# Performance work log

Hardware: AMD Instinct MI355X
Metric: run time of the kernel (lower is better)

The kernel has to match this reference:

```python
import jax, jax.numpy as jnp
import numpy as np
import math

B, T, E, H = 4, 1024, 1024, 16
D = E // H  # head_dim = 64
EPS = 1e-5


def setup_inputs() -> dict:
    key = jax.random.key(0)
    k1, k2, k3 = jax.random.split(key, 3)
    x = jax.random.normal(k1, (B, T, E), dtype=jnp.float32)
    scale = jnp.ones((E,), dtype=jnp.float32)
    w_qkv = jax.random.normal(k2, (3 * E, E), dtype=jnp.float32) * (1.0 / math.sqrt(E))
    w_proj = jax.random.normal(k3, (E, E), dtype=jnp.float32) * (1.0 / math.sqrt(E))
    return {"x": x, "scale": scale, "w_qkv": w_qkv, "w_proj": w_proj}


def reference(x, scale, w_qkv, w_proj):
    # RMSNorm
    xn = x * jax.lax.rsqrt(jnp.mean(x * x, axis=-1, keepdims=True) + EPS) * scale
    # QKV projection (torch Linear: y = x @ W.T)
    qkv = jnp.einsum('bte,fe->btf', xn, w_qkv)  # [B,T,3E]
    q, k, v = jnp.split(qkv, 3, axis=-1)
    # [B,T,E] -> [B,H,T,D]
    q = q.reshape(B, T, H, D).transpose(0, 2, 1, 3)
    k = k.reshape(B, T, H, D).transpose(0, 2, 1, 3)
    v = v.reshape(B, T, H, D).transpose(0, 2, 1, 3)
    # causal attention
    attn = jnp.einsum('bhqd,bhkd->bhqk', q, k) / math.sqrt(D)
    causal = jnp.tril(jnp.ones((T, T), dtype=bool))
    attn = jnp.where(causal, attn, -jnp.inf)
    attn = jax.nn.softmax(attn, axis=-1)
    out = jnp.einsum('bhqk,bhkd->bhqd', attn, v)  # [B,H,T,D]
    out = out.transpose(0, 2, 1, 3).reshape(B, T, E)
    # output projection
    return jnp.einsum('bte,fe->btf', out, w_proj)
```

## Files before the change

### kernel.cpp

```cpp
#include <hip/hip_runtime.h>
#include <hip/hip_bf16.h>
#include <stdint.h>

#define B_SZ 4
#define T_SEQ 1024
#define E_DIM 1024
#define NH 16
#define HD 64
#define THREE_E 3072
#define NTOK 4096

typedef unsigned short u16;
typedef unsigned int u32;
using short8v = __attribute__((ext_vector_type(8))) short;
using short4v = __attribute__((ext_vector_type(4))) short;
using f32x4 = __attribute__((ext_vector_type(4))) float;

__device__ __forceinline__ u16 f2bf(float f) {
    union { float f; uint32_t u; } c; c.f = f;
    uint32_t u = c.u;
    uint32_t r = (u + 0x7FFFu + ((u >> 16) & 1u)) >> 16;
    return (u16)r;
}

__device__ __forceinline__ u32 cvt_pk_bf16(float lo, float hi) {
    u32 r;
    asm("v_cvt_pk_bf16_f32 %0, %1, %2" : "=v"(r) : "v"(lo), "v"(hi));
    return r;
}

__device__ __forceinline__ void gload_lds16(const u16* g, u16* l) {
    __builtin_amdgcn_global_load_lds((const __attribute__((address_space(1))) void*)g,
                                     (__attribute__((address_space(3))) void*)l, 16, 0, 0);
}

__global__ __launch_bounds__(256) void rmsnorm_kernel(const float* __restrict__ x,
                                                      const float* __restrict__ scale,
                                                      u16* __restrict__ xn) {
    int row = blockIdx.x;
    int tid = threadIdx.x;
    const float4* xr = reinterpret_cast<const float4*>(x + (size_t)row * E_DIM);
    float4 v = xr[tid];
    float ss = v.x * v.x + v.y * v.y + v.z * v.z + v.w * v.w;
    for (int off = 32; off > 0; off >>= 1) ss += __shfl_xor(ss, off);
    __shared__ float red[4];
    if ((tid & 63) == 0) red[tid >> 6] = ss;
    __syncthreads();
    float total = red[0] + red[1] + red[2] + red[3];
    float rs = rsqrtf(total * (1.0f / E_DIM) + 1e-5f);
    const float4* sc4 = reinterpret_cast<const float4*>(scale);
    float4 s = sc4[tid];
    u16* o = xn + (size_t)row * E_DIM + tid * 4;
    o[0] = f2bf(v.x * rs * s.x);
    o[1] = f2bf(v.y * rs * s.y);
    o[2] = f2bf(v.z * rs * s.z);
    o[3] = f2bf(v.w * rs * s.w);
}

__global__ __launch_bounds__(256) void cast_weights_kernel(const float* __restrict__ wq,
                                                           const float* __restrict__ wp,
                                                           u16* __restrict__ wqb,
                                                           u16* __restrict__ wpb) {
    const int NQ = (THREE_E * E_DIM) / 4;
    const int NP = (E_DIM * E_DIM) / 4;
    int i = blockIdx.x * 256 + threadIdx.x;
    if (i < NQ) {
        float4 v = reinterpret_cast<const float4*>(wq)[i];
        u16* o = wqb + (size_t)i * 4;
        o[0] = f2bf(v.x); o[1] = f2bf(v.y); o[2] = f2bf(v.z); o[3] = f2bf(v.w);
    } else if (i < NQ + NP) {
        int j = i - NQ;
        float4 v = reinterpret_cast<const float4*>(wp)[j];
        u16* o = wpb + (size_t)j * 4;
        o[0] = f2bf(v.x); o[1] = f2bf(v.y); o[2] = f2bf(v.z); o[3] = f2bf(v.w);
    }
}

template <bool OUT_BF16>
__global__ __launch_bounds__(256) void gemm_lds_kernel(const u16* __restrict__ A,
                                                       const u16* __restrict__ Bw,
                                                       void* __restrict__ C,
                                                       int N, int K) {
    __shared__ u16 As[128 * 64];
    __shared__ u16 Bs[128 * 64];
    int tid = threadIdx.x;
    int lane = tid & 63, wid = tid >> 6;
    int lq = lane & 15, lg = lane >> 4;

    int gx = gridDim.x;
    int nwg = gx * gridDim.y;
    int orig = blockIdx.y * gx + blockIdx.x;
    int cpx = nwg >> 3;
    int swz = (orig & 7) * cpx + (orig >> 3);
    int bx = swz % gx, by = swz / gx;
    int mblk = by * 128, nblk = bx * 128;

    int srow = wid * 32 + (lane >> 3);
    int csw = ((lane & 7) ^ ((lane >> 3) & 7)) * 8;
    const u16* gA = A + (size_t)(mblk + srow) * K + csw;
    const u16* gB = Bw + (size_t)(nblk + srow) * K + csw;
    u16* lA = As + wid * 2048;
    u16* lB = Bs + wid * 2048;

    f32x4 acc[4][4] = {};
    int m0w = (wid >> 1) * 64;
    int n0w = (wid & 1) * 64;
    int r7 = lq & 7;

    for (int k0 = 0; k0 < K; k0 += 64) {
        __syncthreads();
#pragma unroll
        for (int i = 0; i < 4; ++i) gload_lds16(gA + k0 + (size_t)i * 8 * K, lA + i * 512);
#pragma unroll
        for (int i = 0; i < 4; ++i) gload_lds16(gB + k0 + (size_t)i * 8 * K, lB + i * 512);
        __syncthreads();
        short8v af[2][4], bf[2][4];
#pragma unroll
        for (int kk = 0; kk < 2; ++kk) {
#pragma unroll
            for (int mi = 0; mi < 4; ++mi)
                af[kk][mi] = *reinterpret_cast<const short8v*>(
                    &As[(m0w + mi * 16 + lq) * 64 + ((kk * 4 + lg) ^ r7) * 8]);
#pragma unroll
            for (int ni = 0; ni < 4; ++ni)
                bf[kk][ni] = *reinterpret_cast<const short8v*>(
                    &Bs[(n0w + ni * 16 + lq) * 64 + ((kk * 4 + lg) ^ r7) * 8]);
        }
        __builtin_amdgcn_s_setprio(1);
#pragma unroll
        for (int mi = 0; mi < 4; ++mi)
#pragma unroll
            for (int ni = 0; ni < 4; ++ni) {
                acc[mi][ni] = __builtin_amdgcn_mfma_f32_16x16x32_bf16(af[0][mi], bf[0][ni], acc[mi][ni], 0, 0, 0);
                acc[mi][ni] = __builtin_amdgcn_mfma_f32_16x16x32_bf16(af[1][mi], bf[1][ni], acc[mi][ni], 0, 0, 0);
            }
        __builtin_amdgcn_s_setprio(0);
    }
#pragma unroll
    for (int mi = 0; mi < 4; ++mi) {
#pragma unroll
        for (int ni = 0; ni < 4; ++ni) {
#pragma unroll
            for (int j = 0; j < 4; ++j) {
                int row = mblk + m0w + mi * 16 + lg * 4 + j;
                int col = nblk + n0w + ni * 16 + lq;
                float val = acc[mi][ni][j];
                if (OUT_BF16)
                    ((u16*)C)[(size_t)row * N + col] = f2bf(val);
                else
                    ((float*)C)[(size_t)row * N + col] = val;
            }
        }
    }
}

template <bool DIAG>
__device__ __forceinline__ void attn_tile(const u16 (*__restrict__ Kt)[72],
                                          const u16 (*__restrict__ Vt)[72],
                                          const short8v* __restrict__ qf,
                                          f32x4* __restrict__ o,
                                          float& l_r,
                                          int lq, int lg, int wid, int kt64, int qg) {
    const float CLOG = 0.18033688011112042f;
    const float MOFF = 11.541560327111707f;
    int ksmax = DIAG ? wid : 3;
    f32x4 st[4] = {};
    __builtin_amdgcn_s_setprio(1);
#pragma unroll
    for (int ks = 0; ks < 4; ++ks) {
        if (ks <= ksmax) {
            short8v a0 = *reinterpret_cast<const short8v*>(&Kt[ks * 16 + lq][lg * 8]);
            short8v a1 = *reinterpret_cast<const short8v*>(&Kt[ks * 16 + lq][32 + lg * 8]);
            st[ks] = __builtin_amdgcn_mfma_f32_16x16x32_bf16(a0, qf[0], st[ks], 0, 0, 0);
            st[ks] = __builtin_amdgcn_mfma_f32_16x16x32_bf16(a1, qf[1], st[ks], 0, 0, 0);
        }
    }
    __builtin_amdgcn_s_setprio(0);
    float p[4][4];
    float psum = 0.f;
#pragma unroll
    for (int ks = 0; ks < 4; ++ks)
#pragma unroll
        for (int j = 0; j < 4; ++j) {
            float v = st[ks][j];
            if (DIAG) {
                int kg = kt64 + ks * 16 + lg * 4 + j;
                v = (ks <= ksmax && kg <= qg) ? v : -INFINITY;
            }
            float pv = exp2f(fmaf(v, CLOG, -MOFF));
            p[ks][j] = pv;
            psum += pv;
        }
    l_r += psum;
    union { u32 w2[2]; short4v v; } pa[4];
#pragma unroll
    for (int ks = 0; ks < 4; ++ks) {
        pa[ks].w2[0] = cvt_pk_bf16(p[ks][0], p[ks][1]);
        pa[ks].w2[1] = cvt_pk_bf16(p[ks][2], p[ks][3]);
    }
    __builtin_amdgcn_s_setprio(1);
#pragma unroll
    for (int ni = 0; ni < 4; ++ni) {
        int d = ni * 16 + lq;
        int sw = ((d >> 3) & 7) << 3;
        const u16* vrow = Vt[d];
#pragma unroll
        for (int ks = 0; ks < 4; ++ks) {
            if (ks <= ksmax) {
                short4v vb = *reinterpret_cast<const short4v*>(&vrow[(ks * 16 + lg * 4) ^ sw]);
                o[ni] = __builtin_amdgcn_mfma_f32_16x16x16bf16_1k(pa[ks].v, vb, o[ni], 0, 0, 0);
            }
        }
    }
    __builtin_amdgcn_s_setprio(0);
}

__global__ __launch_bounds__(256) void attn_kernel(const u16* __restrict__ qkv,
                                                   u16* __restrict__ out) {
    int tid = threadIdx.x;
    int lane = tid & 63, wid = tid >> 6;
    int lq = lane & 15, lg = lane >> 4;
    int bh = blockIdx.y;
    int b = bh >> 4, h = bh & 15;
    int qlo_blk = blockIdx.x;
    int qhi_blk = 15 - qlo_blk;
    int qt_lo = qlo_blk * 64 + wid * 16;
    int qt_hi = qhi_blk * 64 + wid * 16;

    const u16* base = qkv + (size_t)b * T_SEQ * THREE_E;
    const u16* Qb = base + h * HD;
    const u16* Kb = base + E_DIM + h * HD;

    __shared__ __align__(16) u16 Kt[2][64][72];
    __shared__ __align__(16) u16 Vt[2][64][72];

    short8v qf_lo[2], qf_hi[2];
    {
        const u16* qr = Qb + (size_t)(qt_lo + lq) * THREE_E + lg * 8;
        qf_lo[0] = *reinterpret_cast<const short8v*>(qr);
        qf_lo[1] = *reinterpret_cast<const short8v*>(qr + 32);
        qr = Qb + (size_t)(qt_hi + lq) * THREE_E + lg * 8;
        qf_hi[0] = *reinterpret_cast<const short8v*>(qr);
        qf_hi[1] = *reinterpret_cast<const short8v*>(qr + 32);
    }
    f32x4 o_lo[4] = {}, o_hi[4] = {};
    float l_lo = 0.f, l_hi = 0.f;
    int qg_lo = qt_lo + lq, qg_hi = qt_hi + lq;

    int row_s = tid >> 3, c8 = tid & 7;
    short8v kreg[2], vreg[2];

#pragma unroll
    for (int i = 0; i < 2; ++i) {
        const u16* src = Kb + (size_t)(row_s + i * 32) * THREE_E + c8 * 8;
        kreg[i] = *reinterpret_cast<const short8v*>(src);
        vreg[i] = *reinterpret_cast<const short8v*>(src + E_DIM);
    }
#pragma unroll
    for (int i = 0; i < 2; ++i) {
        int row = row_s + i * 32;
        *reinterpret_cast<short8v*>(&Kt[0][row][c8 * 8]) = kreg[i];
        int rs = row ^ (c8 << 3);
#pragma unroll
        for (int e = 0; e < 8; ++e) Vt[0][c8 * 8 + e][rs] = (u16)vreg[i][e];
    }
    if (qhi_blk >= 1) {
#pragma unroll
        for (int i = 0; i < 2; ++i) {
            const u16* src = Kb + (size_t)(64 + row_s + i * 32) * THREE_E + c8 * 8;
            kreg[i] = *reinterpret_cast<const short8v*>(src);
            vreg[i] = *reinterpret_cast<const short8v*>(src + E_DIM);
        }
    }
    __syncthreads();

    for (int kt = 0; kt <= qhi_blk; ++kt) {
        int cur = kt & 1;
        if (kt < qhi_blk) {
#pragma unroll
            for (int i = 0; i < 2; ++i) {
                int row = row_s + i * 32;
                *reinterpret_cast<short8v*>(&Kt[cur ^ 1][row][c8 * 8]) = kreg[i];
                int rs = row ^ (c8 << 3);
#pragma unroll
                for (int e = 0; e < 8; ++e) Vt[cur ^ 1][c8 * 8 + e][rs] = (u16)vreg[i][e];
            }
            if (kt + 1 < qhi_blk) {
#pragma unroll
                for (int i = 0; i < 2; ++i) {
                    const u16* src = Kb + (size_t)((kt + 2) * 64 + row_s + i * 32) * THREE_E + c8 * 8;
                    kreg[i] = *reinterpret_cast<const short8v*>(src);
                    vreg[i] = *reinterpret_cast<const short8v*>(src + E_DIM);
                }
            }
        }
        if (kt < qlo_blk)
            attn_tile<false>(Kt[cur], Vt[cur], qf_lo, o_lo, l_lo, lq, lg, wid, kt * 64, qg_lo);
        else if (kt == qlo_blk)
            attn_tile<true>(Kt[cur], Vt[cur], qf_lo, o_lo, l_lo, lq, lg, wid, kt * 64, qg_lo);
        if (kt < qhi_blk)
            attn_tile<false>(Kt[cur], Vt[cur], qf_hi, o_hi, l_hi, lq, lg, wid, kt * 64, qg_hi);
        else
            attn_tile<true>(Kt[cur], Vt[cur], qf_hi, o_hi, l_hi, lq, lg, wid, kt * 64, qg_hi);
        __syncthreads();
    }
    float lf_lo = l_lo, lf_hi = l_hi;
    lf_lo += __shfl_xor(lf_lo, 16); lf_lo += __shfl_xor(lf_lo, 32);
    lf_hi += __shfl_xor(lf_hi, 16); lf_hi += __shfl_xor(lf_hi, 32);
#pragma unroll
    for (int j = 0; j < 4; ++j) {
        float linv = 1.0f / __shfl(lf_lo, lg * 4 + j);
        size_t row = (size_t)b * T_SEQ + qt_lo + lg * 4 + j;
#pragma unroll
        for (int ni = 0; ni < 4; ++ni)
            out[row * E_DIM + h * HD + ni * 16 + lq] = f2bf(o_lo[ni][j] * linv);
    }
#pragma unroll
    for (int j = 0; j < 4; ++j) {
        float linv = 1.0f / __shfl(lf_hi, lg * 4 + j);
        size_t row = (size_t)b * T_SEQ + qt_hi + lg * 4 + j;
#pragma unroll
        for (int ni = 0; ni < 4; ++ni)
            out[row * E_DIM + h * HD + ni * 16 + lq] = f2bf(o_hi[ni][j] * linv);
    }
}

extern "C" void kernel_launch(void* const* d_in, const int* in_sizes, int n_in,
                              void* d_out, int out_size, void* d_ws, size_t ws_size,
                              hipStream_t stream) {
    const float* x = (const float*)d_in[0];
    const float* scale = (const float*)d_in[1];
    const float* w_qkv = (const float*)d_in[2];
    const float* w_proj = (const float*)d_in[3];
    float* out = (float*)d_out;

    char* ws = (char*)d_ws;
    u16* xn   = (u16*)(ws);
    u16* wqb  = (u16*)(ws + (8ull << 20));
    u16* wpb  = (u16*)(ws + (14ull << 20));
    u16* qkv  = (u16*)(ws + (16ull << 20));
    u16* aout = (u16*)(ws + (40ull << 20));

    rmsnorm_kernel<<<dim3(NTOK), dim3(256), 0, stream>>>(x, scale, xn);
    cast_weights_kernel<<<dim3(4096), dim3(256), 0, stream>>>(w_qkv, w_proj, wqb, wpb);
    gemm_lds_kernel<true><<<dim3(THREE_E / 128, NTOK / 128), dim3(256), 0, stream>>>(
        xn, wqb, (void*)qkv, THREE_E, E_DIM);
    attn_kernel<<<dim3(8, B_SZ * NH), dim3(256), 0, stream>>>(qkv, aout);
    gemm_lds_kernel<false><<<dim3(E_DIM / 128, NTOK / 128), dim3(256), 0, stream>>>(
        aout, wpb, (void*)out, E_DIM, E_DIM);
}
```

Measured before the change: 98.49 us.

## Fuse prep kernels, split attention across 8 waves, narrow proj GEMM tile

Result: faster. 89.67 us (-9.0%).

```diff
diff --git a/kernel.cpp b/kernel.cpp
--- a/kernel.cpp
+++ b/kernel.cpp
@@ -34,55 +34,57 @@
                                      (__attribute__((address_space(3))) void*)l, 16, 0, 0);
 }
 
-__global__ __launch_bounds__(256) void rmsnorm_kernel(const float* __restrict__ x,
-                                                      const float* __restrict__ scale,
-                                                      u16* __restrict__ xn) {
-    int row = blockIdx.x;
+__global__ __launch_bounds__(256) void prep_kernel(const float* __restrict__ x,
+                                                   const float* __restrict__ scale,
+                                                   const float* __restrict__ wq,
+                                                   const float* __restrict__ wp,
+                                                   u16* __restrict__ xn,
+                                                   u16* __restrict__ wqb,
+                                                   u16* __restrict__ wpb) {
+    int bx = blockIdx.x;
     int tid = threadIdx.x;
-    const float4* xr = reinterpret_cast<const float4*>(x + (size_t)row * E_DIM);
-    float4 v = xr[tid];
-    float ss = v.x * v.x + v.y * v.y + v.z * v.z + v.w * v.w;
-    for (int off = 32; off > 0; off >>= 1) ss += __shfl_xor(ss, off);
-    __shared__ float red[4];
-    if ((tid & 63) == 0) red[tid >> 6] = ss;
-    __syncthreads();
-    float total = red[0] + red[1] + red[2] + red[3];
-    float rs = rsqrtf(total * (1.0f / E_DIM) + 1e-5f);
-    const float4* sc4 = reinterpret_cast<const float4*>(scale);
-    float4 s = sc4[tid];
-    u16* o = xn + (size_t)row * E_DIM + tid * 4;
-    o[0] = f2bf(v.x * rs * s.x);
-    o[1] = f2bf(v.y * rs * s.y);
-    o[2] = f2bf(v.z * rs * s.z);
-    o[3] = f2bf(v.w * rs * s.w);
-}
-
-__global__ __launch_bounds__(256) void cast_weights_kernel(const float* __restrict__ wq,
-                                                           const float* __restrict__ wp,
-                                                           u16* __restrict__ wqb,
-                                                           u16* __restrict__ wpb) {
-    const int NQ = (THREE_E * E_DIM) / 4;
-    const int NP = (E_DIM * E_DIM) / 4;
-    int i = blockIdx.x * 256 + threadIdx.x;
-    if (i < NQ) {
-        float4 v = reinterpret_cast<const float4*>(wq)[i];
-        u16* o = wqb + (size_t)i * 4;
-        o[0] = f2bf(v.x); o[1] = f2bf(v.y); o[2] = f2bf(v.z); o[3] = f2bf(v.w);
-    } else if (i < NQ + NP) {
-        int j = i - NQ;
-        float4 v = reinterpret_cast<const float4*>(wp)[j];
-        u16* o = wpb + (size_t)j * 4;
-        o[0] = f2bf(v.x); o[1] = f2bf(v.y); o[2] = f2bf(v.z); o[3] = f2bf(v.w);
-    }
-}
-
-template <bool OUT_BF16>
+    if (bx < 4096) {
+        int row = bx;
+        const float4* xr = reinterpret_cast<const float4*>(x + (size_t)row * E_DIM);
+        float4 v = xr[tid];
+        float ss = v.x * v.x + v.y * v.y + v.z * v.z + v.w * v.w;
+        for (int off = 32; off > 0; off >>= 1) ss += __shfl_xor(ss, off);
+        __shared__ float red[4];
+        if ((tid & 63) == 0) red[tid >> 6] = ss;
+        __syncthreads();
+        float total = red[0] + red[1] + red[2] + red[3];
+        float rs = rsqrtf(total * (1.0f / E_DIM) + 1e-5f);
+        float4 s = reinterpret_cast<const float4*>(scale)[tid];
+        u16* o = xn + (size_t)row * E_DIM + tid * 4;
+        o[0] = f2bf(v.x * rs * s.x);
+        o[1] = f2bf(v.y * rs * s.y);
+        o[2] = f2bf(v.z * rs * s.z);
+        o[3] = f2bf(v.w * rs * s.w);
+    } else {
+        const int NQ = (THREE_E * E_DIM) / 4;
+        const int NP = (E_DIM * E_DIM) / 4;
+        int i = (bx - 4096) * 256 + tid;
+        if (i < NQ) {
+            float4 v = reinterpret_cast<const float4*>(wq)[i];
+            u16* o = wqb + (size_t)i * 4;
+            o[0] = f2bf(v.x); o[1] = f2bf(v.y); o[2] = f2bf(v.z); o[3] = f2bf(v.w);
+        } else if (i < NQ + NP) {
+            int j = i - NQ;
+            float4 v = reinterpret_cast<const float4*>(wp)[j];
+            u16* o = wpb + (size_t)j * 4;
+            o[0] = f2bf(v.x); o[1] = f2bf(v.y); o[2] = f2bf(v.z); o[3] = f2bf(v.w);
+        }
+    }
+}
+
+template <int BN, bool OUT_BF16>
 __global__ __launch_bounds__(256) void gemm_lds_kernel(const u16* __restrict__ A,
                                                        const u16* __restrict__ Bw,
                                                        void* __restrict__ C,
                                                        int N, int K) {
+    constexpr int NFR = BN / 32;
     __shared__ u16 As[128 * 64];
-    __shared__ u16 Bs[128 * 64];
+    __shared__ u16 Bs[BN * 64];
     int tid = threadIdx.x;
     int lane = tid & 63, wid = tid >> 6;
     int lq = lane & 15, lg = lane >> 4;
@@ -93,18 +95,19 @@
     int cpx = nwg >> 3;
     int swz = (orig & 7) * cpx + (orig >> 3);
     int bx = swz % gx, by = swz / gx;
-    int mblk = by * 128, nblk = bx * 128;
-
-    int srow = wid * 32 + (lane >> 3);
+    int mblk = by * 128, nblk = bx * BN;
+
+    int srowA = wid * 32 + (lane >> 3);
+    int srowB = wid * (BN / 4) + (lane >> 3);
     int csw = ((lane & 7) ^ ((lane >> 3) & 7)) * 8;
-    const u16* gA = A + (size_t)(mblk + srow) * K + csw;
-    const u16* gB = Bw + (size_t)(nblk + srow) * K + csw;
+    const u16* gA = A + (size_t)(mblk + srowA) * K + csw;
+    const u16* gB = Bw + (size_t)(nblk + srowB) * K + csw;
     u16* lA = As + wid * 2048;
-    u16* lB = Bs + wid * 2048;
-
-    f32x4 acc[4][4] = {};
+    u16* lB = Bs + wid * (BN / 4) * 64;
+
+    f32x4 acc[4][NFR] = {};
     int m0w = (wid >> 1) * 64;
-    int n0w = (wid & 1) * 64;
+    int n0w = (wid & 1) * (BN / 2);
     int r7 = lq & 7;
 
     for (int k0 = 0; k0 < K; k0 += 64) {
@@ -112,9 +115,9 @@
 #pragma unroll
         for (int i = 0; i < 4; ++i) gload_lds16(gA + k0 + (size_t)i * 8 * K, lA + i * 512);
 #pragma unroll
-        for (int i = 0; i < 4; ++i) gload_lds16(gB + k0 + (size_t)i * 8 * K, lB + i * 512);
+        for (int i = 0; i < NFR; ++i) gload_lds16(gB + k0 + (size_t)i * 8 * K, lB + i * 512);
         __syncthreads();
-        short8v af[2][4], bf[2][4];
+        short8v af[2][4], bf[2][NFR];
 #pragma unroll
         for (int kk = 0; kk < 2; ++kk) {
 #pragma unroll
@@ -122,7 +125,7 @@
                 af[kk][mi] = *reinterpret_cast<const short8v*>(
                     &As[(m0w + mi * 16 + lq) * 64 + ((kk * 4 + lg) ^ r7) * 8]);
 #pragma unroll
-            for (int ni = 0; ni < 4; ++ni)
+            for (int ni = 0; ni < NFR; ++ni)
                 bf[kk][ni] = *reinterpret_cast<const short8v*>(
                     &Bs[(n0w + ni * 16 + lq) * 64 + ((kk * 4 + lg) ^ r7) * 8]);
         }
@@ -130,7 +133,7 @@
 #pragma unroll
         for (int mi = 0; mi < 4; ++mi)
 #pragma unroll
-            for (int ni = 0; ni < 4; ++ni) {
+            for (int ni = 0; ni < NFR; ++ni) {
                 acc[mi][ni] = __builtin_amdgcn_mfma_f32_16x16x32_bf16(af[0][mi], bf[0][ni], acc[mi][ni], 0, 0, 0);
                 acc[mi][ni] = __builtin_amdgcn_mfma_f32_16x16x32_bf16(af[1][mi], bf[1][ni], acc[mi][ni], 0, 0, 0);
             }
@@ -139,7 +142,7 @@
 #pragma unroll
     for (int mi = 0; mi < 4; ++mi) {
 #pragma unroll
-        for (int ni = 0; ni < 4; ++ni) {
+        for (int ni = 0; ni < NFR; ++ni) {
 #pragma unroll
             for (int j = 0; j < 4; ++j) {
                 int row = mblk + m0w + mi * 16 + lg * 4 + j;
@@ -160,10 +163,10 @@
                                           const short8v* __restrict__ qf,
                                           f32x4* __restrict__ o,
                                           float& l_r,
-                                          int lq, int lg, int wid, int kt64, int qg) {
+                                          int lq, int lg, int w4, int kt64, int qg) {
     const float CLOG = 0.18033688011112042f;
     const float MOFF = 11.541560327111707f;
-    int ksmax = DIAG ? wid : 3;
+    int ksmax = DIAG ? w4 : 3;
     f32x4 st[4] = {};
     __builtin_amdgcn_s_setprio(1);
 #pragma unroll
@@ -215,17 +218,19 @@
     __builtin_amdgcn_s_setprio(0);
 }
 
-__global__ __launch_bounds__(256) void attn_kernel(const u16* __restrict__ qkv,
+__global__ __launch_bounds__(512) void attn_kernel(const u16* __restrict__ qkv,
                                                    u16* __restrict__ out) {
     int tid = threadIdx.x;
     int lane = tid & 63, wid = tid >> 6;
     int lq = lane & 15, lg = lane >> 4;
+    int w4 = wid & 3;
+    bool is_hi = wid >= 4;
     int bh = blockIdx.y;
     int b = bh >> 4, h = bh & 15;
     int qlo_blk = blockIdx.x;
     int qhi_blk = 15 - qlo_blk;
-    int qt_lo = qlo_blk * 64 + wid * 16;
-    int qt_hi = qhi_blk * 64 + wid * 16;
+    int myblk = is_hi ? qhi_blk : qlo_blk;
+    int qt = myblk * 64 + w4 * 16;
 
     const u16* base = qkv + (size_t)b * T_SEQ * THREE_E;
     const u16* Qb = base + h * HD;
@@ -234,94 +239,72 @@
     __shared__ __align__(16) u16 Kt[2][64][72];
     __shared__ __align__(16) u16 Vt[2][64][72];
 
-    short8v qf_lo[2], qf_hi[2];
+    short8v qf[2];
     {
-        const u16* qr = Qb + (size_t)(qt_lo + lq) * THREE_E + lg * 8;
-        qf_lo[0] = *reinterpret_cast<const short8v*>(qr);
-        qf_lo[1] = *reinterpret_cast<const short8v*>(qr + 32);
-        qr = Qb + (size_t)(qt_hi + lq) * THREE_E + lg * 8;
-        qf_hi[0] = *reinterpret_cast<const short8v*>(qr);
-        qf_hi[1] = *reinterpret_cast<const short8v*>(qr + 32);
-    }
-    f32x4 o_lo[4] = {}, o_hi[4] = {};
-    float l_lo = 0.f, l_hi = 0.f;
-    int qg_lo = qt_lo + lq, qg_hi = qt_hi + lq;
+        const u16* qr = Qb + (size_t)(qt + lq) * THREE_E + lg * 8;
+        qf[0] = *reinterpret_cast<const short8v*>(qr);
+        qf[1] = *reinterpret_cast<const short8v*>(qr + 32);
+    }
+    f32x4 o[4] = {};
+    float l_r = 0.f;
+    int qg = qt + lq;
 
     int row_s = tid >> 3, c8 = tid & 7;
-    short8v kreg[2], vreg[2];
-
-#pragma unroll
-    for (int i = 0; i < 2; ++i) {
-        const u16* src = Kb + (size_t)(row_s + i * 32) * THREE_E + c8 * 8;
-        kreg[i] = *reinterpret_cast<const short8v*>(src);
-        vreg[i] = *reinterpret_cast<const short8v*>(src + E_DIM);
-    }
-#pragma unroll
-    for (int i = 0; i < 2; ++i) {
-        int row = row_s + i * 32;
-        *reinterpret_cast<short8v*>(&Kt[0][row][c8 * 8]) = kreg[i];
-        int rs = row ^ (c8 << 3);
-#pragma unroll
-        for (int e = 0; e < 8; ++e) Vt[0][c8 * 8 + e][rs] = (u16)vreg[i][e];
+    short8v kreg, vreg;
+
+    {
+        const u16* src = Kb + (size_t)row_s * THREE_E + c8 * 8;
+        kreg = *reinterpret_cast<const short8v*>(src);
+        vreg = *reinterpret_cast<const short8v*>(src + E_DIM);
+    }
+    {
+        *reinterpret_cast<short8v*>(&Kt[0][row_s][c8 * 8]) = kreg;
+        int rs = row_s ^ (c8 << 3);
+#pragma unroll
+        for (int e = 0; e < 8; ++e) Vt[0][c8 * 8 + e][rs] = (u16)vreg[e];
     }
     if (qhi_blk >= 1) {
-#pragma unroll
-        for (int i = 0; i < 2; ++i) {
-            const u16* src = Kb + (size_t)(64 + row_s + i * 32) * THREE_E + c8 * 8;
-            kreg[i] = *reinterpret_cast<const short8v*>(src);
-            vreg[i] = *reinterpret_cast<const short8v*>(src + E_DIM);
-        }
+        const u16* src = Kb + (size_t)(64 + row_s) * THREE_E + c8 * 8;
+        kreg = *reinterpret_cast<const short8v*>(src);
+        vreg = *reinterpret_cast<const short8v*>(src + E_DIM);
     }
     __syncthreads();
 
     for (int kt = 0; kt <= qhi_blk; ++kt) {
         int cur = kt & 1;
         if (kt < qhi_blk) {
-#pragma unroll
-            for (int i = 0; i < 2; ++i) {
-                int row = row_s + i * 32;
-                *reinterpret_cast<short8v*>(&Kt[cur ^ 1][row][c8 * 8]) = kreg[i];
-                int rs = row ^ (c8 << 3);
-#pragma unroll
-                for (int e = 0; e < 8; ++e) Vt[cur ^ 1][c8 * 8 + e][rs] = (u16)vreg[i][e];
-            }
+            *reinterpret_cast<short8v*>(&Kt[cur ^ 1][row_s][c8 * 8]) = kreg;
+            int rs = row_s ^ (c8 << 3);
+#pragma unroll
+            for (int e = 0; e < 8; ++e) Vt[cur ^ 1][c8 * 8 + e][rs] = (u16)vreg[e];
             if (kt + 1 < qhi_blk) {
-#pragma unroll
-                for (int i = 0; i < 2; ++i) {
-                    const u16* src = Kb + (size_t)((kt + 2) * 64 + row_s + i * 32) * THREE_E + c8 * 8;
-                    kreg[i] = *reinterpret_cast<const short8v*>(src);
-                    vreg[i] = *reinterpret_cast<const short8v*>(src + E_DIM);
-                }
-            }
-        }
-        if (kt < qlo_blk)
-            attn_tile<false>(Kt[cur], Vt[cur], qf_lo, o_lo, l_lo, lq, lg, wid, kt * 64, qg_lo);
-        else if (kt == qlo_blk)
-            attn_tile<true>(Kt[cur], Vt[cur], qf_lo, o_lo, l_lo, lq, lg, wid, kt * 64, qg_lo);
-        if (kt < qhi_blk)
-            attn_tile<false>(Kt[cur], Vt[cur], qf_hi, o_hi, l_hi, lq, lg, wid, kt * 64, qg_hi);
-        else
-            attn_tile<true>(Kt[cur], Vt[cur], qf_hi, o_hi, l_hi, lq, lg, wid, kt * 64, qg_hi);
+                const u16* src = Kb + (size_t)((kt + 2) * 64 + row_s) * THREE_E + c8 * 8;
+                kreg = *reinterpret_cast<const short8v*>(src);
+                vreg = *reinterpret_cast<const short8v*>(src + E_DIM);
+            }
+        }
+        if (is_hi) {
+            if (kt < qhi_blk)
+                attn_tile<false>(Kt[cur], Vt[cur], qf, o, l_r, lq, lg, w4, kt * 64, qg);
+            else
+                attn_tile<true>(Kt[cur], Vt[cur], qf, o, l_r, lq, lg, w4, kt * 64, qg);
+        } else {
+            if (kt < qlo_blk)
+                attn_tile<false>(Kt[cur], Vt[cur], qf, o, l_r, lq, lg, w4, kt * 64, qg);
+            else if (kt == qlo_blk)
+                attn_tile<true>(Kt[cur], Vt[cur], qf, o, l_r, lq, lg, w4, kt * 64, qg);
+        }
         __syncthreads();
     }
-    float lf_lo = l_lo, lf_hi = l_hi;
-    lf_lo += __shfl_xor(lf_lo, 16); lf_lo += __shfl_xor(lf_lo, 32);
-    lf_hi += __shfl_xor(lf_hi, 16); lf_hi += __shfl_xor(lf_hi, 32);
+    float lf = l_r;
+    lf += __shfl_xor(lf, 16); lf += __shfl_xor(lf, 32);
 #pragma unroll
     for (int j = 0; j < 4; ++j) {
-        float linv = 1.0f / __shfl(lf_lo, lg * 4 + j);
-        size_t row = (size_t)b * T_SEQ + qt_lo + lg * 4 + j;
+        float linv = 1.0f / __shfl(lf, lg * 4 + j);
+        size_t row = (size_t)b * T_SEQ + qt + lg * 4 + j;
 #pragma unroll
         for (int ni = 0; ni < 4; ++ni)
-            out[row * E_DIM + h * HD + ni * 16 + lq] = f2bf(o_lo[ni][j] * linv);
-    }
-#pragma unroll
-    for (int j = 0; j < 4; ++j) {
-        float linv = 1.0f / __shfl(lf_hi, lg * 4 + j);
-        size_t row = (size_t)b * T_SEQ + qt_hi + lg * 4 + j;
-#pragma unroll
-        for (int ni = 0; ni < 4; ++ni)
-            out[row * E_DIM + h * HD + ni * 16 + lq] = f2bf(o_hi[ni][j] * linv);
+            out[row * E_DIM + h * HD + ni * 16 + lq] = f2bf(o[ni][j] * linv);
     }
 }
 
@@ -341,11 +324,10 @@
     u16* qkv  = (u16*)(ws + (16ull << 20));
     u16* aout = (u16*)(ws + (40ull << 20));
 
-    rmsnorm_kernel<<<dim3(NTOK), dim3(256), 0, stream>>>(x, scale, xn);
-    cast_weights_kernel<<<dim3(4096), dim3(256), 0, stream>>>(w_qkv, w_proj, wqb, wpb);
-    gemm_lds_kernel<true><<<dim3(THREE_E / 128, NTOK / 128), dim3(256), 0, stream>>>(
+    prep_kernel<<<dim3(8192), dim3(256), 0, stream>>>(x, scale, w_qkv, w_proj, xn, wqb, wpb);
+    gemm_lds_kernel<128, true><<<dim3(THREE_E / 128, NTOK / 128), dim3(256), 0, stream>>>(
         xn, wqb, (void*)qkv, THREE_E, E_DIM);
-    attn_kernel<<<dim3(8, B_SZ * NH), dim3(256), 0, stream>>>(qkv, aout);
-    gemm_lds_kernel<false><<<dim3(E_DIM / 128, NTOK / 128), dim3(256), 0, stream>>>(
+    attn_kernel<<<dim3(8, B_SZ * NH), dim3(512), 0, stream>>>(qkv, aout);
+    gemm_lds_kernel<64, false><<<dim3(E_DIM / 64, NTOK / 128), dim3(256), 0, stream>>>(
         aout, wpb, (void*)out, E_DIM, E_DIM);
 }
```
